# Kernel tuning notes

Hardware: AMD Instinct MI355X
Metric: run time of the kernel (lower is better)

Reference implementation:

```python
import jax, jax.numpy as jnp
import numpy as np

B, S, D, H, F = 64, 512, 1024, 1024, 1024  # note: module requires H == D
EPS = 1e-6


def setup_inputs() -> dict:
    key = jax.random.key(0)
    ks = jax.random.split(key, 14)
    p = lambda k, shape: 0.02 * jax.random.normal(k, shape, dtype=jnp.float32)
    return {
        "hidden_state": jax.random.normal(ks[0], (B, S, D), dtype=jnp.float32),
        "field_hidden_state": jax.random.normal(ks[1], (B, S, F), dtype=jnp.float32),
        "input": jax.random.normal(ks[2], (B, D), dtype=jnp.float32),
        "finished": jnp.zeros((B, 1), dtype=bool),
        "W1": p(ks[3], (H, D)), "b1": p(ks[4], (H,)),
        "W2": p(ks[5], (H, D)), "b2": p(ks[6], (H,)),
        "W3": p(ks[7], (H, 2 * D)), "b3": p(ks[8], (H,)),
        "W4": p(ks[9], (H, F)), "b4": p(ks[10], (H,)),
        "W5": p(ks[11], (H, D)), "b5": p(ks[12], (H,)),
    }


def _norm_over_seq(w):
    # manual exp/max/sum softmax over seq dim (axis 0) with 1e-6 guard, as in torch
    w = jnp.exp(w - jnp.max(w, axis=0, keepdims=True))
    return w / (EPS + jnp.sum(w, axis=0, keepdims=True))


def reference(hidden_state, field_hidden_state, input, finished,
              W1, b1, W2, b2, W3, b3, W4, b4, W5, b5):
    hs = jnp.transpose(hidden_state, (1, 0, 2))        # [S, B, D]
    fs = jnp.transpose(field_hidden_state, (1, 0, 2))  # [S, B, F]
    phi_h = jnp.tanh(hs @ W1.T + b1)                   # [S, B, H]
    phi_f = jnp.tanh(fs @ W4.T + b4)                   # [S, B, H]

    gamma_h = jnp.tanh(input @ W2.T + b2)              # [B, H]
    weights = _norm_over_seq(jnp.sum(phi_h * gamma_h, axis=2, keepdims=True))  # [S, B, 1]

    alpha_h = jnp.tanh(input @ W5.T + b5)              # [B, H]
    field_w = _norm_over_seq(jnp.sum(phi_f * alpha_h, axis=2, keepdims=True))  # [S, B, 1]

    wf = weights * field_w
    weights = wf / (EPS + jnp.sum(wf, axis=0, keepdims=True))  # [S, B, 1]

    context = jnp.sum(hs * weights, axis=0)            # [B, D]
    out = jnp.concatenate([context, input], axis=-1) @ W3.T + b3  # [B, H]
    out = jnp.where(finished, jnp.zeros_like(out), out)
    return out, weights
```

## Files before the change

kernel.cpp:

```cpp
#include <hip/hip_runtime.h>

#define EPS 1e-6f

typedef _Float16 f16;
typedef __fp16 h16x2 __attribute__((ext_vector_type(2)));
typedef _Float16 f16x4 __attribute__((ext_vector_type(4)));
typedef _Float16 f16x8 __attribute__((ext_vector_type(8)));
typedef float f32x4 __attribute__((ext_vector_type(4)));

__device__ __forceinline__ float tanh_fast(float x) {
    float e = __expf(2.0f * x);
    return 1.0f - 2.0f / (e + 1.0f);
}

__global__ __launch_bounds__(256) void wconv_kernel(
    const float* __restrict__ W1, const float* __restrict__ W4,
    f16* __restrict__ W1h, f16* __restrict__ W4h)
{
    int gid = blockIdx.x * 256 + threadIdx.x;
    const float4* s1 = (const float4*)W1;
    const float4* s4 = (const float4*)W4;
    f16x4* d1 = (f16x4*)W1h;
    f16x4* d4 = (f16x4*)W4h;
    #pragma unroll
    for (int r = 0; r < 2; ++r) {
        int i = gid + r * 131072;
        float4 v = s1[i];
        f16x4 o; o[0]=(f16)v.x; o[1]=(f16)v.y; o[2]=(f16)v.z; o[3]=(f16)v.w;
        d1[i] = o;
        float4 u = s4[i];
        f16x4 p; p[0]=(f16)u.x; p[1]=(f16)u.y; p[2]=(f16)u.z; p[3]=(f16)u.w;
        d4[i] = p;
    }
}

__global__ __launch_bounds__(256) void gamal_kernel(
    const float* __restrict__ inp,
    const float* __restrict__ W2, const float* __restrict__ b2,
    const float* __restrict__ W5, const float* __restrict__ b5,
    float* __restrict__ gamm, float* __restrict__ alph)
{
    const float* W  = blockIdx.y ? W5 : W2;
    const float* bs = blockIdx.y ? b5 : b2;
    float* dst      = blockIdx.y ? alph : gamm;
    int wid = threadIdx.x >> 6, lane = threadIdx.x & 63;
    int p = blockIdx.x * 4 + wid;
    int b = p >> 10, h = p & 1023;
    const float4* wr = (const float4*)(W + (size_t)h * 1024);
    const float4* xr = (const float4*)(inp + (size_t)b * 1024);
    float acc = 0.f;
    #pragma unroll
    for (int j = 0; j < 4; ++j) {
        float4 w4 = wr[lane + 64 * j];
        float4 x4 = xr[lane + 64 * j];
        acc += w4.x * x4.x + w4.y * x4.y + w4.z * x4.z + w4.w * x4.w;
    }
    #pragma unroll
    for (int o = 32; o; o >>= 1) acc += __shfl_xor(acc, o);
    if (lane == 0) dst[p] = tanh_fast(acc + bs[h]);
}

__global__ __launch_bounds__(512, 2) void gemm_logits_kernel(
    const float* __restrict__ Ahid, const float* __restrict__ Afld,
    const f16* __restrict__ W1h, const f16* __restrict__ W4h,
    const float* __restrict__ b1, const float* __restrict__ b4,
    const float* __restrict__ gamm, const float* __restrict__ alph,
    float* __restrict__ Lpart)
{
    __shared__ __align__(16) char smA[2][32768];
    __shared__ __align__(16) char smW[2][32768];
    __shared__ float rowpart[256][4];

    const int lin = blockIdx.x;
    const int swz = (lin & 7) * 128 + (lin >> 3);
    const int mat = swz >> 9;
    const int rem = swz & 511;
    const int m_blk = rem >> 2;
    const int nc = rem & 3;
    const int m0 = m_blk << 8;
    const int hc0 = nc << 8;

    const float* A  = mat ? Afld : Ahid;
    const f16*  W   = mat ? W4h : W1h;
    const float* bv = mat ? b4 : b1;
    const float* gv = mat ? alph : gamm;

    const int t = threadIdx.x;
    const int lane = t & 63;
    const int wv = t >> 6;
    const int wr = wv >> 2;
    const int wc = wv & 3;
    const int c16 = lane & 15;
    const int kg = lane >> 4;

    const int srow = t >> 1;
    const int shalf = t & 1;
    const float* aRow = A + (size_t)(m0 + srow) * 1024 + shalf * 32;

    const int lrow = lane >> 3, lslot = lane & 7;
    const int kchunk = lslot ^ lrow;

    const int swzr = (c16 & 7) << 4;
    const int aoffb = (wr * 128 + c16) * 128;
    const int woffb = (wc * 64 + c16) * 128;
    const int kg16 = kg * 16;

    f32x4 acc[8][4];
    #pragma unroll
    for (int i = 0; i < 8; ++i)
        #pragma unroll
        for (int j = 0; j < 4; ++j) acc[i][j] = (f32x4){0.f, 0.f, 0.f, 0.f};

    float4 a_ld[8];

    auto loadA = [&](int kt) {
        const float4* ap = (const float4*)(aRow + kt * 64);
        #pragma unroll
        for (int j = 0; j < 8; ++j) a_ld[j] = ap[j];
    };
    auto writeA = [&](char* buf) {
        char* ad = buf + srow * 128;
        const int swzw = (srow & 7) << 4;
        const int wb = shalf * 64;
        #pragma unroll
        for (int j = 0; j < 4; ++j) {
            union { f16x8 v; h16x2 h[4]; } u;
            float4 x = a_ld[2 * j], y = a_ld[2 * j + 1];
            u.h[0] = __builtin_amdgcn_cvt_pkrtz(x.x, x.y);
            u.h[1] = __builtin_amdgcn_cvt_pkrtz(x.z, x.w);
            u.h[2] = __builtin_amdgcn_cvt_pkrtz(y.x, y.y);
            u.h[3] = __builtin_amdgcn_cvt_pkrtz(y.z, y.w);
            *(f16x8*)(ad + ((wb + j * 16) ^ swzw)) = u.v;
        }
    };
    auto gloadW = [&](int kt, char* buf) {
        #pragma unroll
        for (int j = 0; j < 4; ++j) {
            int r = wv * 32 + j * 8;
            const f16* src = W + (size_t)(hc0 + r + lrow) * 1024 + kt * 64 + kchunk * 8;
            char* dst = buf + r * 128;
            __builtin_amdgcn_global_load_lds(
                (const __attribute__((address_space(1))) void*)src,
                (__attribute__((address_space(3))) void*)dst, 16, 0, 0);
        }
    };

    loadA(0);
    gloadW(0, smW[0]);
    writeA(smA[0]);
    loadA(1);
    asm volatile("s_waitcnt vmcnt(8) lgkmcnt(0)" ::: "memory");
    __builtin_amdgcn_sched_barrier(0);
    __builtin_amdgcn_s_barrier();
    __builtin_amdgcn_sched_barrier(0);

    int cur = 0;
    for (int kt = 0; kt < 16; ++kt) {
        const int ktn  = kt < 15 ? kt + 1 : 15;
        const int ktnn = kt < 14 ? kt + 2 : 15;
        char* aC = smA[cur];
        char* wC = smW[cur];
        char* aN = smA[cur ^ 1];
        char* wN = smW[cur ^ 1];

        gloadW(ktn, wN);

        {
            f16x8 af[8], wf[4];
            const int ko = kg16 ^ swzr;
            #pragma unroll
            for (int mi = 0; mi < 8; ++mi) af[mi] = *(const f16x8*)(aC + aoffb + mi * 2048 + ko);
            #pragma unroll
            for (int ni = 0; ni < 4; ++ni) wf[ni] = *(const f16x8*)(wC + woffb + ni * 2048 + ko);
            __builtin_amdgcn_s_setprio(1);
            #pragma unroll
            for (int ni = 0; ni < 4; ++ni)
                #pragma unroll
                for (int mi = 0; mi < 8; ++mi)
                    acc[mi][ni] = __builtin_amdgcn_mfma_f32_16x16x32_f16(af[mi], wf[ni], acc[mi][ni], 0, 0, 0);
            __builtin_amdgcn_s_setprio(0);
        }

        f16x8 af1[8], wf1[4];
        {
            const int ko = (64 + kg16) ^ swzr;
            #pragma unroll
            for (int mi = 0; mi < 8; ++mi) af1[mi] = *(const f16x8*)(aC + aoffb + mi * 2048 + ko);
            #pragma unroll
            for (int ni = 0; ni < 4; ++ni) wf1[ni] = *(const f16x8*)(wC + woffb + ni * 2048 + ko);
        }

        writeA(aN);
        loadA(ktnn);

        __builtin_amdgcn_s_setprio(1);
        #pragma unroll
        for (int ni = 0; ni < 4; ++ni)
            #pragma unroll
            for (int mi = 0; mi < 8; ++mi)
                acc[mi][ni] = __builtin_amdgcn_mfma_f32_16x16x32_f16(af1[mi], wf1[ni], acc[mi][ni], 0, 0, 0);
        __builtin_amdgcn_s_setprio(0);

        asm volatile("s_waitcnt vmcnt(8) lgkmcnt(0)" ::: "memory");
        __builtin_amdgcn_sched_barrier(0);
        __builtin_amdgcn_s_barrier();
        __builtin_amdgcn_sched_barrier(0);
        cur ^= 1;
    }

    const int bidx = m_blk >> 1;
    float g[4], bb[4];
    #pragma unroll
    for (int ni = 0; ni < 4; ++ni) {
        int h = hc0 + wc * 64 + ni * 16 + c16;
        g[ni]  = gv[(bidx << 10) + h];
        bb[ni] = bv[h];
    }
    #pragma unroll
    for (int mi = 0; mi < 8; ++mi) {
        #pragma unroll
        for (int q = 0; q < 4; ++q) {
            float v = tanh_fast(acc[mi][0][q] + bb[0]) * g[0]
                    + tanh_fast(acc[mi][1][q] + bb[1]) * g[1]
                    + tanh_fast(acc[mi][2][q] + bb[2]) * g[2]
                    + tanh_fast(acc[mi][3][q] + bb[3]) * g[3];
            v += __shfl_xor(v, 1);
            v += __shfl_xor(v, 2);
            v += __shfl_xor(v, 4);
            v += __shfl_xor(v, 8);
            if (c16 == 0)
                rowpart[wr * 128 + mi * 16 + kg * 4 + q][wc] = v;
        }
    }
    __syncthreads();
    if (t < 256)
        Lpart[(size_t)(mat * 4 + nc) * 32768 + m0 + t] =
            rowpart[t][0] + rowpart[t][1] + rowpart[t][2] + rowpart[t][3];
}

__device__ __forceinline__ float blockMax(float v, float* sm) {
    #pragma unroll
    for (int o = 32; o; o >>= 1) v = fmaxf(v, __shfl_xor(v, o));
    if ((threadIdx.x & 63) == 0) sm[threadIdx.x >> 6] = v;
    __syncthreads();
    v = fmaxf(fmaxf(sm[0], sm[1]), fmaxf(sm[2], sm[3]));
    __syncthreads();
    return v;
}
__device__ __forceinline__ float blockSum(float v, float* sm) {
    #pragma unroll
    for (int o = 32; o; o >>= 1) v += __shfl_xor(v, o);
    if ((threadIdx.x & 63) == 0) sm[threadIdx.x >> 6] = v;
    __syncthreads();
    v = sm[0] + sm[1] + sm[2] + sm[3];
    __syncthreads();
    return v;
}

__global__ __launch_bounds__(256) void softmax_combine_kernel(
    const float* __restrict__ Lp,
    float* __restrict__ wfin, float* __restrict__ dout)
{
    __shared__ float sm[4];
    int b = blockIdx.x, t = threadIdx.x;
    float h0 = 0.f, h1 = 0.f, f0 = 0.f, f1 = 0.f;
    #pragma unroll
    for (int nc = 0; nc < 4; ++nc) {
        h0 += Lp[nc * 32768 + b * 512 + t];
        h1 += Lp[nc * 32768 + b * 512 + 256 + t];
        f0 += Lp[(4 + nc) * 32768 + b * 512 + t];
        f1 += Lp[(4 + nc) * 32768 + b * 512 + 256 + t];
    }
    float mh = blockMax(fmaxf(h0, h1), sm);
    float mf = blockMax(fmaxf(f0, f1), sm);
    float e0 = __expf(h0 - mh), e1 = __expf(h1 - mh);
    float q0 = __expf(f0 - mf), q1 = __expf(f1 - mf);
    float sh = blockSum(e0 + e1, sm);
    float sf = blockSum(q0 + q1, sm);
    float wh0 = e0 / (EPS + sh), wh1 = e1 / (EPS + sh);
    float wq0 = q0 / (EPS + sf), wq1 = q1 / (EPS + sf);
    float c0 = wh0 * wq0, c1 = wh1 * wq1;
    float sc = blockSum(c0 + c1, sm);
    float r0 = c0 / (EPS + sc), r1 = c1 / (EPS + sc);
    wfin[b * 512 + t]       = r0;
    wfin[b * 512 + 256 + t] = r1;
    dout[65536 + t * 64 + b]         = r0;
    dout[65536 + (256 + t) * 64 + b] = r1;
}

__global__ __launch_bounds__(256) void context_kernel(
    const float* __restrict__ hs, const float* __restrict__ wgt,
    float* __restrict__ ctxpart)
{
    int dq = blockIdx.x;
    int b  = blockIdx.y;
    int sh = blockIdx.z;
    int t = threadIdx.x;
    int ss = t >> 6, ds = t & 63;
    __shared__ float4 part[4][64];
    const float4* hp = (const float4*)hs;
    float ax = 0.f, ay = 0.f, az = 0.f, aw = 0.f;
    int sBase = sh * 256 + ss * 64;
    for (int i = 0; i < 64; ++i) {
        int s = sBase + i;
        float w = wgt[b * 512 + s];
        float4 v = hp[(size_t)(b * 512 + s) * 256 + dq * 64 + ds];
        ax += v.x * w; ay += v.y * w; az += v.z * w; aw += v.w * w;
    }
    float4 r; r.x = ax; r.y = ay; r.z = az; r.w = aw;
    part[ss][ds] = r;
    __syncthreads();
    if (ss == 0) {
        float4 a0 = part[0][ds], a1 = part[1][ds], a2 = part[2][ds], a3 = part[3][ds];
        float4 o;
        o.x = a0.x + a1.x + a2.x + a3.x;
        o.y = a0.y + a1.y + a2.y + a3.y;
        o.z = a0.z + a1.z + a2.z + a3.z;
        o.w = a0.w + a1.w + a2.w + a3.w;
        ((float4*)ctxpart)[(size_t)sh * 16384 + b * 256 + dq * 64 + ds] = o;
    }
}

__global__ __launch_bounds__(256) void out_kernel(
    const float* __restrict__ ctxpart, const float* __restrict__ inp,
    const float* __restrict__ W3, const float* __restrict__ b3,
    const unsigned char* __restrict__ fin, float* __restrict__ out)
{
    int t = threadIdx.x, wid = t >> 6, lane = t & 63;
    int h = blockIdx.x * 4 + wid;
    __shared__ __align__(16) float xs[2048];
    float4* xsv = (float4*)xs;
    float4 wreg[8];
    const float4* w3r = (const float4*)(W3 + (size_t)h * 2048);
    #pragma unroll
    for (int j = 0; j < 8; ++j) wreg[j] = w3r[lane + 64 * j];
    const float4* cp = (const float4*)ctxpart;
    const float4* xp = (const float4*)inp;
    for (int b = 0; b < 64; ++b) {
        __syncthreads();
        {
            float4 c0 = cp[b * 256 + t];
            float4 c1 = cp[16384 + b * 256 + t];
            float4 cc; cc.x = c0.x + c1.x; cc.y = c0.y + c1.y;
            cc.z = c0.z + c1.z; cc.w = c0.w + c1.w;
            xsv[t] = cc;
            xsv[256 + t] = xp[b * 256 + t];
        }
        __syncthreads();
        float acc = 0.f;
        #pragma unroll
        for (int j = 0; j < 8; ++j) {
            float4 x = xsv[lane + 64 * j];
            acc += wreg[j].x * x.x + wreg[j].y * x.y + wreg[j].z * x.z + wreg[j].w * x.w;
        }
        #pragma unroll
        for (int o = 32; o; o >>= 1) acc += __shfl_xor(acc, o);
        if (lane == 0) out[b * 1024 + h] = fin[b] ? 0.f : (acc + b3[h]);
    }
}

extern "C" void kernel_launch(void* const* d_in, const int* in_sizes, int n_in,
                              void* d_out, int out_size, void* d_ws, size_t ws_size,
                              hipStream_t stream)
{
    const float* hidden = (const float*)d_in[0];
    const float* field  = (const float*)d_in[1];
    const float* input  = (const float*)d_in[2];
    const unsigned char* fin = (const unsigned char*)d_in[3];
    const float* W1 = (const float*)d_in[4];
    const float* b1 = (const float*)d_in[5];
    const float* W2 = (const float*)d_in[6];
    const float* b2 = (const float*)d_in[7];
    const float* W3 = (const float*)d_in[8];
    const float* b3 = (const float*)d_in[9];
    const float* W4 = (const float*)d_in[10];
    const float* b4 = (const float*)d_in[11];
    const float* W5 = (const float*)d_in[12];
    const float* b5 = (const float*)d_in[13];
    float* out = (float*)d_out;

    char* ws = (char*)d_ws;
    float* Lpart = (float*)(ws);
    float* wfin  = (float*)(ws + 1048576);
    float* gamm  = (float*)(ws + 1179648);
    float* alph  = (float*)(ws + 1441792);
    float* ctxp  = (float*)(ws + 1703936);
    f16*   W1h   = (f16*)(ws + 2228224);
    f16*   W4h   = (f16*)(ws + 4325376);

    wconv_kernel<<<512, 256, 0, stream>>>(W1, W4, W1h, W4h);
    gamal_kernel<<<dim3(16384, 2), 256, 0, stream>>>(input, W2, b2, W5, b5, gamm, alph);
    gemm_logits_kernel<<<1024, 512, 0, stream>>>(hidden, field, W1h, W4h,
                                                 b1, b4, gamm, alph, Lpart);
    softmax_combine_kernel<<<64, 256, 0, stream>>>(Lpart, wfin, out);
    context_kernel<<<dim3(4, 64, 2), 256, 0, stream>>>(hidden, wfin, ctxp);
    out_kernel<<<256, 256, 0, stream>>>(ctxp, input, W3, b3, fin, out);
}
```

Before: 382.7 us.

## Pre-convert activations to fp16 and simplify GEMM to single-buffered 128x128 tiles

Adds separate conversion passes that turn hidden and field states (and W1/W4) into fp16 buffers, then feeds the logits GEMM with direct global-to-LDS loads of fp16 A instead of in-kernel fp32 loads and conversion. The GEMM tile shrinks to 128x128 with 256 threads and a single-buffered, barrier-synchronised loop, with partial logits split over 8 column chunks. The context kernel reads the fp16 hidden copy. This adds a full extra write and read of the activations and drops the software pipeline, and it reduces the precision of the context sum.

```diff
diff --git a/kernel.cpp b/kernel.cpp
--- a/kernel.cpp
+++ b/kernel.cpp
@@ -3,7 +3,6 @@
 #define EPS 1e-6f
 
 typedef _Float16 f16;
-typedef __fp16 h16x2 __attribute__((ext_vector_type(2)));
 typedef _Float16 f16x4 __attribute__((ext_vector_type(4)));
 typedef _Float16 f16x8 __attribute__((ext_vector_type(8)));
 typedef float f32x4 __attribute__((ext_vector_type(4)));
@@ -13,24 +12,14 @@
     return 1.0f - 2.0f / (e + 1.0f);
 }
 
-__global__ __launch_bounds__(256) void wconv_kernel(
-    const float* __restrict__ W1, const float* __restrict__ W4,
-    f16* __restrict__ W1h, f16* __restrict__ W4h)
-{
-    int gid = blockIdx.x * 256 + threadIdx.x;
-    const float4* s1 = (const float4*)W1;
-    const float4* s4 = (const float4*)W4;
-    f16x4* d1 = (f16x4*)W1h;
-    f16x4* d4 = (f16x4*)W4h;
-    #pragma unroll
-    for (int r = 0; r < 2; ++r) {
-        int i = gid + r * 131072;
-        float4 v = s1[i];
+__global__ __launch_bounds__(256) void conv_kernel(
+    const float4* __restrict__ src, f16x4* __restrict__ dst, int n4)
+{
+    int stride = gridDim.x * 256;
+    for (int i = blockIdx.x * 256 + threadIdx.x; i < n4; i += stride) {
+        float4 v = src[i];
         f16x4 o; o[0]=(f16)v.x; o[1]=(f16)v.y; o[2]=(f16)v.z; o[3]=(f16)v.w;
-        d1[i] = o;
-        float4 u = s4[i];
-        f16x4 p; p[0]=(f16)u.x; p[1]=(f16)u.y; p[2]=(f16)u.z; p[3]=(f16)u.w;
-        d4[i] = p;
+        dst[i] = o;
     }
 }
 
@@ -60,155 +49,90 @@
     if (lane == 0) dst[p] = tanh_fast(acc + bs[h]);
 }
 
-__global__ __launch_bounds__(512, 2) void gemm_logits_kernel(
-    const float* __restrict__ Ahid, const float* __restrict__ Afld,
-    const f16* __restrict__ W1h, const f16* __restrict__ W4h,
+__global__ __launch_bounds__(256, 4) void gemm_logits_kernel(
+    const f16* __restrict__ Ah,
+    const f16* __restrict__ Wh,
     const float* __restrict__ b1, const float* __restrict__ b4,
     const float* __restrict__ gamm, const float* __restrict__ alph,
     float* __restrict__ Lpart)
 {
-    __shared__ __align__(16) char smA[2][32768];
-    __shared__ __align__(16) char smW[2][32768];
-    __shared__ float rowpart[256][4];
+    __shared__ __align__(16) char smA[16384];
+    __shared__ __align__(16) char smW[16384];
+    __shared__ float rowpart[128][2];
 
     const int lin = blockIdx.x;
-    const int swz = (lin & 7) * 128 + (lin >> 3);
-    const int mat = swz >> 9;
-    const int rem = swz & 511;
-    const int m_blk = rem >> 2;
-    const int nc = rem & 3;
-    const int m0 = m_blk << 8;
-    const int hc0 = nc << 8;
-
-    const float* A  = mat ? Afld : Ahid;
-    const f16*  W   = mat ? W4h : W1h;
+    const int gidx = (lin & 7) * 512 + (lin >> 3);
+    const int mat = gidx >> 11;
+    const int rem = gidx & 2047;
+    const int m_blk = rem >> 3;
+    const int nc = rem & 7;
+    const int m0 = m_blk << 7;
+    const int hc0 = nc << 7;
+    const int bidx = m_blk >> 2;
+
+    const f16* A   = Ah + (size_t)mat * 33554432;
+    const f16* W   = Wh + (size_t)mat * 1048576;
     const float* bv = mat ? b4 : b1;
     const float* gv = mat ? alph : gamm;
 
     const int t = threadIdx.x;
     const int lane = t & 63;
     const int wv = t >> 6;
-    const int wr = wv >> 2;
-    const int wc = wv & 3;
+    const int wr = wv >> 1;
+    const int wc = wv & 1;
     const int c16 = lane & 15;
     const int kg = lane >> 4;
 
-    const int srow = t >> 1;
-    const int shalf = t & 1;
-    const float* aRow = A + (size_t)(m0 + srow) * 1024 + shalf * 32;
-
     const int lrow = lane >> 3, lslot = lane & 7;
     const int kchunk = lslot ^ lrow;
 
     const int swzr = (c16 & 7) << 4;
-    const int aoffb = (wr * 128 + c16) * 128;
+    const int aoffb = (wr * 64 + c16) * 128;
     const int woffb = (wc * 64 + c16) * 128;
     const int kg16 = kg * 16;
 
-    f32x4 acc[8][4];
-    #pragma unroll
-    for (int i = 0; i < 8; ++i)
+    f32x4 acc[4][4];
+    #pragma unroll
+    for (int i = 0; i < 4; ++i)
         #pragma unroll
         for (int j = 0; j < 4; ++j) acc[i][j] = (f32x4){0.f, 0.f, 0.f, 0.f};
 
-    float4 a_ld[8];
-
-    auto loadA = [&](int kt) {
-        const float4* ap = (const float4*)(aRow + kt * 64);
-        #pragma unroll
-        for (int j = 0; j < 8; ++j) a_ld[j] = ap[j];
-    };
-    auto writeA = [&](char* buf) {
-        char* ad = buf + srow * 128;
-        const int swzw = (srow & 7) << 4;
-        const int wb = shalf * 64;
-        #pragma unroll
-        for (int j = 0; j < 4; ++j) {
-            union { f16x8 v; h16x2 h[4]; } u;
-            float4 x = a_ld[2 * j], y = a_ld[2 * j + 1];
-            u.h[0] = __builtin_amdgcn_cvt_pkrtz(x.x, x.y);
-            u.h[1] = __builtin_amdgcn_cvt_pkrtz(x.z, x.w);
-            u.h[2] = __builtin_amdgcn_cvt_pkrtz(y.x, y.y);
-            u.h[3] = __builtin_amdgcn_cvt_pkrtz(y.z, y.w);
-            *(f16x8*)(ad + ((wb + j * 16) ^ swzw)) = u.v;
-        }
-    };
-    auto gloadW = [&](int kt, char* buf) {
+    for (int kt = 0; kt < 16; ++kt) {
         #pragma unroll
         for (int j = 0; j < 4; ++j) {
             int r = wv * 32 + j * 8;
-            const f16* src = W + (size_t)(hc0 + r + lrow) * 1024 + kt * 64 + kchunk * 8;
-            char* dst = buf + r * 128;
+            const f16* srcA = A + (size_t)(m0 + r + lrow) * 1024 + kt * 64 + kchunk * 8;
             __builtin_amdgcn_global_load_lds(
-                (const __attribute__((address_space(1))) void*)src,
-                (__attribute__((address_space(3))) void*)dst, 16, 0, 0);
-        }
-    };
-
-    loadA(0);
-    gloadW(0, smW[0]);
-    writeA(smA[0]);
-    loadA(1);
-    asm volatile("s_waitcnt vmcnt(8) lgkmcnt(0)" ::: "memory");
-    __builtin_amdgcn_sched_barrier(0);
-    __builtin_amdgcn_s_barrier();
-    __builtin_amdgcn_sched_barrier(0);
-
-    int cur = 0;
-    for (int kt = 0; kt < 16; ++kt) {
-        const int ktn  = kt < 15 ? kt + 1 : 15;
-        const int ktnn = kt < 14 ? kt + 2 : 15;
-        char* aC = smA[cur];
-        char* wC = smW[cur];
-        char* aN = smA[cur ^ 1];
-        char* wN = smW[cur ^ 1];
-
-        gloadW(ktn, wN);
-
-        {
-            f16x8 af[8], wf[4];
-            const int ko = kg16 ^ swzr;
+                (const __attribute__((address_space(1))) void*)srcA,
+                (__attribute__((address_space(3))) void*)(smA + r * 128), 16, 0, 0);
+        }
+        #pragma unroll
+        for (int j = 0; j < 4; ++j) {
+            int r = wv * 32 + j * 8;
+            const f16* srcW = W + (size_t)(hc0 + r + lrow) * 1024 + kt * 64 + kchunk * 8;
+            __builtin_amdgcn_global_load_lds(
+                (const __attribute__((address_space(1))) void*)srcW,
+                (__attribute__((address_space(3))) void*)(smW + r * 128), 16, 0, 0);
+        }
+        __syncthreads();
+
+        #pragma unroll
+        for (int kk = 0; kk < 2; ++kk) {
+            const int ko = (kk * 64 + kg16) ^ swzr;
+            f16x8 af[4], wf[4];
             #pragma unroll
-            for (int mi = 0; mi < 8; ++mi) af[mi] = *(const f16x8*)(aC + aoffb + mi * 2048 + ko);
+            for (int i = 0; i < 4; ++i) af[i] = *(const f16x8*)(smA + aoffb + i * 2048 + ko);
             #pragma unroll
-            for (int ni = 0; ni < 4; ++ni) wf[ni] = *(const f16x8*)(wC + woffb + ni * 2048 + ko);
-            __builtin_amdgcn_s_setprio(1);
+            for (int i = 0; i < 4; ++i) wf[i] = *(const f16x8*)(smW + woffb + i * 2048 + ko);
             #pragma unroll
             for (int ni = 0; ni < 4; ++ni)
                 #pragma unroll
-                for (int mi = 0; mi < 8; ++mi)
+                for (int mi = 0; mi < 4; ++mi)
                     acc[mi][ni] = __builtin_amdgcn_mfma_f32_16x16x32_f16(af[mi], wf[ni], acc[mi][ni], 0, 0, 0);
-            __builtin_amdgcn_s_setprio(0);
-        }
-
-        f16x8 af1[8], wf1[4];
-        {
-            const int ko = (64 + kg16) ^ swzr;
-            #pragma unroll
-            for (int mi = 0; mi < 8; ++mi) af1[mi] = *(const f16x8*)(aC + aoffb + mi * 2048 + ko);
-            #pragma unroll
-            for (int ni = 0; ni < 4; ++ni) wf1[ni] = *(const f16x8*)(wC + woffb + ni * 2048 + ko);
-        }
-
-        writeA(aN);
-        loadA(ktnn);
-
-        __builtin_amdgcn_s_setprio(1);
-        #pragma unroll
-        for (int ni = 0; ni < 4; ++ni)
-            #pragma unroll
-            for (int mi = 0; mi < 8; ++mi)
-                acc[mi][ni] = __builtin_amdgcn_mfma_f32_16x16x32_f16(af1[mi], wf1[ni], acc[mi][ni], 0, 0, 0);
-        __builtin_amdgcn_s_setprio(0);
-
-        asm volatile("s_waitcnt vmcnt(8) lgkmcnt(0)" ::: "memory");
-        __builtin_amdgcn_sched_barrier(0);
-        __builtin_amdgcn_s_barrier();
-        __builtin_amdgcn_sched_barrier(0);
-        cur ^= 1;
-    }
-
-    const int bidx = m_blk >> 1;
+        }
+        __syncthreads();
+    }
+
     float g[4], bb[4];
     #pragma unroll
     for (int ni = 0; ni < 4; ++ni) {
@@ -217,7 +141,7 @@
         bb[ni] = bv[h];
     }
     #pragma unroll
-    for (int mi = 0; mi < 8; ++mi) {
+    for (int mi = 0; mi < 4; ++mi) {
         #pragma unroll
         for (int q = 0; q < 4; ++q) {
             float v = tanh_fast(acc[mi][0][q] + bb[0]) * g[0]
@@ -229,13 +153,12 @@
             v += __shfl_xor(v, 4);
             v += __shfl_xor(v, 8);
             if (c16 == 0)
-                rowpart[wr * 128 + mi * 16 + kg * 4 + q][wc] = v;
-        }
-    }
-    __syncthreads();
-    if (t < 256)
-        Lpart[(size_t)(mat * 4 + nc) * 32768 + m0 + t] =
-            rowpart[t][0] + rowpart[t][1] + rowpart[t][2] + rowpart[t][3];
+                rowpart[wr * 64 + mi * 16 + kg * 4 + q][wc] = v;
+        }
+    }
+    __syncthreads();
+    if (t < 128)
+        Lpart[(size_t)(mat * 8 + nc) * 32768 + m0 + t] = rowpart[t][0] + rowpart[t][1];
 }
 
 __device__ __forceinline__ float blockMax(float v, float* sm) {
@@ -265,11 +188,11 @@
     int b = blockIdx.x, t = threadIdx.x;
     float h0 = 0.f, h1 = 0.f, f0 = 0.f, f1 = 0.f;
     #pragma unroll
-    for (int nc = 0; nc < 4; ++nc) {
+    for (int nc = 0; nc < 8; ++nc) {
         h0 += Lp[nc * 32768 + b * 512 + t];
         h1 += Lp[nc * 32768 + b * 512 + 256 + t];
-        f0 += Lp[(4 + nc) * 32768 + b * 512 + t];
-        f1 += Lp[(4 + nc) * 32768 + b * 512 + 256 + t];
+        f0 += Lp[(8 + nc) * 32768 + b * 512 + t];
+        f1 += Lp[(8 + nc) * 32768 + b * 512 + 256 + t];
     }
     float mh = blockMax(fmaxf(h0, h1), sm);
     float mf = blockMax(fmaxf(f0, f1), sm);
@@ -289,7 +212,7 @@
 }
 
 __global__ __launch_bounds__(256) void context_kernel(
-    const float* __restrict__ hs, const float* __restrict__ wgt,
+    const f16* __restrict__ Ah, const float* __restrict__ wgt,
     float* __restrict__ ctxpart)
 {
     int dq = blockIdx.x;
@@ -297,27 +220,26 @@
     int sh = blockIdx.z;
     int t = threadIdx.x;
     int ss = t >> 6, ds = t & 63;
-    __shared__ float4 part[4][64];
-    const float4* hp = (const float4*)hs;
-    float ax = 0.f, ay = 0.f, az = 0.f, aw = 0.f;
+    __shared__ float part[4][64][8];
+    float a[8] = {0,0,0,0,0,0,0,0};
     int sBase = sh * 256 + ss * 64;
+    const f16* hp = Ah + (size_t)b * 524288 + dq * 512 + ds * 8;
     for (int i = 0; i < 64; ++i) {
         int s = sBase + i;
         float w = wgt[b * 512 + s];
-        float4 v = hp[(size_t)(b * 512 + s) * 256 + dq * 64 + ds];
-        ax += v.x * w; ay += v.y * w; az += v.z * w; aw += v.w * w;
-    }
-    float4 r; r.x = ax; r.y = ay; r.z = az; r.w = aw;
-    part[ss][ds] = r;
+        f16x8 v = *(const f16x8*)(hp + (size_t)s * 1024);
+        #pragma unroll
+        for (int j = 0; j < 8; ++j) a[j] += w * (float)v[j];
+    }
+    #pragma unroll
+    for (int j = 0; j < 8; ++j) part[ss][ds][j] = a[j];
     __syncthreads();
     if (ss == 0) {
-        float4 a0 = part[0][ds], a1 = part[1][ds], a2 = part[2][ds], a3 = part[3][ds];
-        float4 o;
-        o.x = a0.x + a1.x + a2.x + a3.x;
-        o.y = a0.y + a1.y + a2.y + a3.y;
-        o.z = a0.z + a1.z + a2.z + a3.z;
-        o.w = a0.w + a1.w + a2.w + a3.w;
-        ((float4*)ctxpart)[(size_t)sh * 16384 + b * 256 + dq * 64 + ds] = o;
+        #pragma unroll
+        for (int j = 0; j < 8; ++j) {
+            float o = part[0][ds][j] + part[1][ds][j] + part[2][ds][j] + part[3][ds][j];
+            ctxpart[(size_t)sh * 65536 + b * 1024 + dq * 512 + ds * 8 + j] = o;
+        }
     }
 }
 
@@ -381,18 +303,21 @@
 
     char* ws = (char*)d_ws;
     float* Lpart = (float*)(ws);
-    float* wfin  = (float*)(ws + 1048576);
-    float* gamm  = (float*)(ws + 1179648);
-    float* alph  = (float*)(ws + 1441792);
-    float* ctxp  = (float*)(ws + 1703936);
-    f16*   W1h   = (f16*)(ws + 2228224);
-    f16*   W4h   = (f16*)(ws + 4325376);
-
-    wconv_kernel<<<512, 256, 0, stream>>>(W1, W4, W1h, W4h);
+    float* wfin  = (float*)(ws + 2097152);
+    float* gamm  = (float*)(ws + 2228224);
+    float* alph  = (float*)(ws + 2490368);
+    float* ctxp  = (float*)(ws + 2752512);
+    f16*   Wh    = (f16*)(ws + 3276800);
+    f16*   Ah    = (f16*)(ws + 7471104);
+
+    conv_kernel<<<4096, 256, 0, stream>>>((const float4*)hidden, (f16x4*)Ah, 8388608);
+    conv_kernel<<<4096, 256, 0, stream>>>((const float4*)field,  (f16x4*)(Ah + 33554432), 8388608);
+    conv_kernel<<<1024, 256, 0, stream>>>((const float4*)W1, (f16x4*)Wh, 262144);
+    conv_kernel<<<1024, 256, 0, stream>>>((const float4*)W4, (f16x4*)(Wh + 1048576), 262144);
+
     gamal_kernel<<<dim3(16384, 2), 256, 0, stream>>>(input, W2, b2, W5, b5, gamm, alph);
-    gemm_logits_kernel<<<1024, 512, 0, stream>>>(hidden, field, W1h, W4h,
-                                                 b1, b4, gamm, alph, Lpart);
+    gemm_logits_kernel<<<4096, 256, 0, stream>>>(Ah, Wh, b1, b4, gamm, alph, Lpart);
     softmax_combine_kernel<<<64, 256, 0, stream>>>(Lpart, wfin, out);
-    context_kernel<<<dim3(4, 64, 2), 256, 0, stream>>>(hidden, wfin, ctxp);
+    context_kernel<<<dim3(2, 64, 2), 256, 0, stream>>>(Ah, wfin, ctxp);
     out_kernel<<<256, 256, 0, stream>>>(ctxp, input, W3, b3, fin, out);
 }
```

Measured after the change: 344.3 us. -10.0%, faster.
